# Kernel optimization log

Hardware: AMD Instinct MI355X
Metric: run time of the kernel (lower is better)

Reference implementation:

```python
import jax, jax.numpy as jnp
import numpy as np

NEG_SLOPE = 0.01  # F.leaky_relu / nn.LeakyReLU default

def _leaky(x):
    return jnp.where(x >= 0, x, NEG_SLOPE * x)

def _cgconv(x, src, dst, edge_attr, Wf, bf, Ws, bs):
    # PyG CGConv: z = [x_i, x_j, e]; msg = sigmoid(lin_f(z)) * softplus(lin_s(z)); out = x + scatter_add(msg, i)
    z = jnp.concatenate([x[dst], x[src], edge_attr], axis=-1)  # [E, 2C+D]
    m = jax.nn.sigmoid(z @ Wf + bf) * jax.nn.softplus(z @ Ws + bs)  # [E, C]
    agg = jax.ops.segment_sum(m, dst, num_segments=x.shape[0])
    return x + agg

def setup_inputs() -> dict:
    key = jax.random.key(0)
    ks = jax.random.split(key, 16)
    N, E, C, D, NC, G = 50000, 800000, 128, 32, 10, 64
    inp = {}
    inp['x'] = jax.random.normal(ks[0], (N, C), dtype=jnp.float32)
    inp['y'] = jax.random.randint(ks[1], (G,), 0, NC)
    inp['edge_index'] = jax.random.randint(ks[2], (2, E), 0, N)
    inp['edge_attr'] = jax.random.normal(ks[3], (E, D), dtype=jnp.float32)
    inp['batch'] = jnp.sort(jax.random.randint(ks[4], (N,), 0, G))
    s = 0.05
    inp['lin_W'] = jax.random.normal(ks[5], (C + NC, C), dtype=jnp.float32) * s
    inp['lin_b'] = jnp.zeros((C,), dtype=jnp.float32)
    inp['c1_Wf'] = jax.random.normal(ks[6], (2 * C + D, C), dtype=jnp.float32) * s
    inp['c1_bf'] = jnp.zeros((C,), dtype=jnp.float32)
    inp['c1_Ws'] = jax.random.normal(ks[7], (2 * C + D, C), dtype=jnp.float32) * s
    inp['c1_bs'] = jnp.zeros((C,), dtype=jnp.float32)
    inp['c2_Wf'] = jax.random.normal(ks[8], (2 * C + D, C), dtype=jnp.float32) * s
    inp['c2_bf'] = jnp.zeros((C,), dtype=jnp.float32)
    inp['c2_Ws'] = jax.random.normal(ks[9], (2 * C + D, C), dtype=jnp.float32) * s
    inp['c2_bs'] = jnp.zeros((C,), dtype=jnp.float32)
    inp['fc1_W'] = jax.random.normal(ks[10], (C + NC, 32), dtype=jnp.float32) * s
    inp['fc1_b'] = jnp.zeros((32,), dtype=jnp.float32)
    inp['fc2_W'] = jax.random.normal(ks[11], (32, 1), dtype=jnp.float32) * s
    inp['fc2_b'] = jnp.zeros((1,), dtype=jnp.float32)
    return inp

def reference(x, y, edge_index, edge_attr, batch, lin_W, lin_b, c1_Wf, c1_bf, c1_Ws, c1_bs, c2_Wf, c2_bf, c2_Ws, c2_bs, fc1_W, fc1_b, fc2_W, fc2_b):
    NC = fc1_W.shape[0] - c1_Wf.shape[1]  # n_classes = 10
    G = y.shape[0]
    src, dst = edge_index[0], edge_index[1]
    one_hot = jax.nn.one_hot(y[batch], NC, dtype=x.dtype)  # [N, NC]
    h = _leaky(jnp.concatenate([x, one_hot], axis=1) @ lin_W + lin_b)
    h = _leaky(_cgconv(h, src, dst, edge_attr, c1_Wf, c1_bf, c1_Ws, c1_bs))
    h = _cgconv(h, src, dst, edge_attr, c2_Wf, c2_bf, c2_Ws, c2_bs)
    h = jnp.concatenate([h, one_hot], axis=1)  # [N, C+NC]
    sums = jax.ops.segment_sum(h, batch, num_segments=G)
    cnts = jax.ops.segment_sum(jnp.ones((h.shape[0],), h.dtype), batch, num_segments=G)
    pooled = sums / jnp.maximum(cnts, 1.0)[:, None]  # global_mean_pool
    out = _leaky(pooled @ fc1_W + fc1_b) @ fc2_W + fc2_b
    return jax.nn.sigmoid(out)
```

## Files before the change

kernel.cpp:

```cpp
#include <hip/hip_runtime.h>
#include <hip/hip_bf16.h>
#include <math.h>

#define CCH 128
#define DK  32
#define NCLS 10

typedef __attribute__((ext_vector_type(2))) float f32x2;

__device__ __forceinline__ float leaky_f(float v) { return v >= 0.f ? v : 0.01f * v; }

__device__ __forceinline__ f32x2 gate2(f32x2 gf, f32x2 gs) {
  float sgx = 1.f / (1.f + __expf(-gf.x));
  float sgy = 1.f / (1.f + __expf(-gf.y));
  float spx = fmaxf(gs.x, 0.f) + __logf(1.f + __expf(-fabsf(gs.x)));
  float spy = fmaxf(gs.y, 0.f) + __logf(1.f + __expf(-fabsf(gs.y)));
  f32x2 r = {sgx * spx, sgy * spy};
  return r;
}

__global__ void k_hist(const int* __restrict__ dst, int* __restrict__ cnt, int E) {
  int e = blockIdx.x * 256 + threadIdx.x;
  if (e < E) atomicAdd(&cnt[dst[e]], 1);
}

__global__ void k_scan(const int* __restrict__ cnt, int* __restrict__ off,
                       int* __restrict__ cur, int N) {
  __shared__ int wsum[16];
  __shared__ int carry_s;
  int t = threadIdx.x;
  int lane = t & 63, w = t >> 6;
  if (t == 0) carry_s = 0;
  __syncthreads();
  for (int base = 0; base < N; base += 1024) {
    int i = base + t;
    int carry = carry_s;
    int v = (i < N) ? cnt[i] : 0;
    int s = v;
    #pragma unroll
    for (int d = 1; d < 64; d <<= 1) {
      int tmp = __shfl_up(s, d);
      if (lane >= d) s += tmp;
    }
    if (lane == 63) wsum[w] = s;
    __syncthreads();
    if (t < 16) {
      int u = wsum[t];
      #pragma unroll
      for (int d = 1; d < 16; d <<= 1) {
        int tmp = __shfl_up(u, d);
        if (t >= d) u += tmp;
      }
      wsum[t] = u;
      if (t == 15) carry_s = carry + u;
    }
    __syncthreads();
    int wbase = carry + (w > 0 ? wsum[w - 1] : 0);
    int excl = wbase + s - v;
    if (i < N) { off[i] = excl; cur[i] = excl; }
    __syncthreads();
  }
  if (t == 0) off[N] = carry_s;
}

__global__ void k_fill(const int* __restrict__ dst, const int* __restrict__ srcArr,
                       int* __restrict__ cur, int* __restrict__ eid,
                       int* __restrict__ esrc, int E) {
  int e = blockIdx.x * 256 + threadIdx.x;
  if (e < E) {
    int p = atomicAdd(&cur[dst[e]], 1);
    eid[p] = e;
    esrc[p] = srcArr[e];
  }
}

__global__ void k_gea(const int* __restrict__ eid, const float* __restrict__ ea,
                      float* __restrict__ ea_csr, int E) {
  int t = blockIdx.x * 256 + threadIdx.x;
  if (t >= E * 8) return;
  int i = t >> 3, q = t & 7;
  int e = eid[i];
  *(float4*)&ea_csr[(size_t)i * DK + q * 4] =
      *(const float4*)&ea[(size_t)e * DK + q * 4];
}

__global__ __launch_bounds__(256) void k_embed(
    const float* __restrict__ x, const float* __restrict__ lin_W,
    const float* __restrict__ lin_b, const int* __restrict__ batch,
    const int* __restrict__ y, float* __restrict__ h, int M) {
  __shared__ float Al[32 * 128];
  __shared__ float Wl[32 * 128];
  int t = threadIdx.x;
  int row0 = blockIdx.x * 32;
  for (int i = t * 4; i < 32 * 128; i += 1024) {
    int r = i >> 7, k = i & 127;
    int gr = row0 + r;
    float4 v = {0.f, 0.f, 0.f, 0.f};
    if (gr < M) v = *(const float4*)&x[(size_t)gr * 128 + k];
    *(float4*)&Al[i] = v;
  }
  int c4 = (t & 31) * 4;
  int rb = (t >> 5) * 4;
  float acc[4][4] = {};
  for (int ks = 0; ks < 128; ks += 32) {
    __syncthreads();
    for (int i = t * 4; i < 32 * 128; i += 1024)
      *(float4*)&Wl[i] = *(const float4*)&lin_W[(size_t)ks * 128 + i];
    __syncthreads();
    for (int k = 0; k < 32; k += 4) {
      float4 a[4];
      #pragma unroll
      for (int r = 0; r < 4; ++r) a[r] = *(float4*)&Al[(rb + r) * 128 + ks + k];
      #pragma unroll
      for (int kk = 0; kk < 4; ++kk) {
        float4 w = *(float4*)&Wl[(k + kk) * 128 + c4];
        #pragma unroll
        for (int r = 0; r < 4; ++r) {
          float av = kk == 0 ? a[r].x : kk == 1 ? a[r].y : kk == 2 ? a[r].z : a[r].w;
          acc[r][0] = fmaf(av, w.x, acc[r][0]);
          acc[r][1] = fmaf(av, w.y, acc[r][1]);
          acc[r][2] = fmaf(av, w.z, acc[r][2]);
          acc[r][3] = fmaf(av, w.w, acc[r][3]);
        }
      }
    }
  }
  #pragma unroll
  for (int r = 0; r < 4; ++r) {
    int gr = row0 + rb + r;
    if (gr < M) {
      int cls = y[batch[gr]];
      const float* wrow = &lin_W[(size_t)(128 + cls) * 128];
      float4 o;
      o.x = leaky_f(acc[r][0] + lin_b[c4 + 0] + wrow[c4 + 0]);
      o.y = leaky_f(acc[r][1] + lin_b[c4 + 1] + wrow[c4 + 1]);
      o.z = leaky_f(acc[r][2] + lin_b[c4 + 2] + wrow[c4 + 2]);
      o.w = leaky_f(acc[r][3] + lin_b[c4 + 3] + wrow[c4 + 3]);
      *(float4*)&h[(size_t)gr * 128 + c4] = o;
    }
  }
}

__global__ __launch_bounds__(256) void k_proj(
    const float* __restrict__ h, const float* __restrict__ Wf,
    const float* __restrict__ Ws, float* __restrict__ P, int M) {
  __shared__ float Al[32 * 128];
  __shared__ float Wl[32 * 128];
  int t = threadIdx.x;
  int part = blockIdx.y;
  const float* Wsrc = (part < 2 ? Wf : Ws) + (size_t)(part & 1) * (128 * 128);
  int row0 = blockIdx.x * 32;
  for (int i = t * 4; i < 32 * 128; i += 1024) {
    int r = i >> 7, k = i & 127;
    int gr = row0 + r;
    float4 v = {0.f, 0.f, 0.f, 0.f};
    if (gr < M) v = *(const float4*)&h[(size_t)gr * 128 + k];
    *(float4*)&Al[i] = v;
  }
  int c4 = (t & 31) * 4;
  int rb = (t >> 5) * 4;
  float acc[4][4] = {};
  for (int ks = 0; ks < 128; ks += 32) {
    __syncthreads();
    for (int i = t * 4; i < 32 * 128; i += 1024)
      *(float4*)&Wl[i] = *(const float4*)&Wsrc[(size_t)ks * 128 + i];
    __syncthreads();
    for (int k = 0; k < 32; k += 4) {
      float4 a[4];
      #pragma unroll
      for (int r = 0; r < 4; ++r) a[r] = *(float4*)&Al[(rb + r) * 128 + ks + k];
      #pragma unroll
      for (int kk = 0; kk < 4; ++kk) {
        float4 w = *(float4*)&Wl[(k + kk) * 128 + c4];
        #pragma unroll
        for (int r = 0; r < 4; ++r) {
          float av = kk == 0 ? a[r].x : kk == 1 ? a[r].y : kk == 2 ? a[r].z : a[r].w;
          acc[r][0] = fmaf(av, w.x, acc[r][0]);
          acc[r][1] = fmaf(av, w.y, acc[r][1]);
          acc[r][2] = fmaf(av, w.z, acc[r][2]);
          acc[r][3] = fmaf(av, w.w, acc[r][3]);
        }
      }
    }
  }
  #pragma unroll
  for (int r = 0; r < 4; ++r) {
    int gr = row0 + rb + r;
    if (gr < M) {
      float4 o = {acc[r][0], acc[r][1], acc[r][2], acc[r][3]};
      *(float4*)&P[(size_t)gr * 512 + part * 128 + c4] = o;
    }
  }
}

__global__ __launch_bounds__(256, 8)
void k_agg(
    const float* __restrict__ hin, const float* __restrict__ P,
    const int* __restrict__ off,
    const int* __restrict__ esrcArr, const float* __restrict__ ea_csr,
    const float* __restrict__ Wf, const float* __restrict__ Ws,
    const float* __restrict__ bfv, const float* __restrict__ bsv,
    float* __restrict__ hout, int N, int do_leaky) {
  __shared__ float WlF[32 * 128];
  __shared__ float WlS[32 * 128];
  int t = threadIdx.x;
  for (int i = t * 4; i < 32 * 128; i += 1024) {
    *(float4*)&WlF[i] = *(const float4*)&Wf[(size_t)256 * 128 + i];
    *(float4*)&WlS[i] = *(const float4*)&Ws[(size_t)256 * 128 + i];
  }
  __syncthreads();
  int lane = t & 63;
  int wave = __builtin_amdgcn_readfirstlane(t >> 6);
  int gw = blockIdx.x * 4 + wave;
  int c2 = lane * 2;
  f32x2 bf2 = *(const f32x2*)&bfv[c2];
  f32x2 bs2 = *(const f32x2*)&bsv[c2];
  int nstreams = gridDim.x * 4;
  for (int n = gw; n < N; n += nstreams) {
    int i0 = __builtin_amdgcn_readfirstlane(off[n]);
    int i1 = __builtin_amdgcn_readfirstlane(off[n + 1]);
    f32x2 acc = *(const f32x2*)&hin[(size_t)n * 128 + c2];
    f32x2 gf0 = *(const f32x2*)&P[(size_t)n * 512 + c2] + bf2;
    f32x2 gs0 = *(const f32x2*)&P[(size_t)n * 512 + 256 + c2] + bs2;
    #pragma unroll 1
    for (int i = i0; i < i1; ++i) {
      int s = __builtin_amdgcn_readfirstlane(esrcArr[i]);
      f32x2 gf = gf0 + *(const f32x2*)&P[(size_t)s * 512 + 128 + c2];
      f32x2 gs = gs0 + *(const f32x2*)&P[(size_t)s * 512 + 384 + c2];
      const float* e0 = ea_csr + (size_t)i * DK;
      #pragma unroll
      for (int q = 0; q < 4; ++q) {
        float4 a = *(const float4*)&e0[q * 8];
        float4 b = *(const float4*)&e0[q * 8 + 4];
        float ekk[8] = {a.x, a.y, a.z, a.w, b.x, b.y, b.z, b.w};
        #pragma unroll
        for (int j = 0; j < 8; ++j) {
          int k = q * 8 + j;
          f32x2 wfk = *(const f32x2*)&WlF[k * 128 + c2];
          f32x2 wsk = *(const f32x2*)&WlS[k * 128 + c2];
          f32x2 e2 = {ekk[j], ekk[j]};
          gf += e2 * wfk;
          gs += e2 * wsk;
        }
      }
      acc += gate2(gf, gs);
    }
    if (do_leaky) { acc.x = leaky_f(acc.x); acc.y = leaky_f(acc.y); }
    *(f32x2*)&hout[(size_t)n * 128 + c2] = acc;
  }
}

__device__ __forceinline__ int lbound(const int* a, int n, int key) {
  int lo = 0, hi = n;
  while (lo < hi) { int m = (lo + hi) >> 1; if (a[m] < key) lo = m + 1; else hi = m; }
  return lo;
}

__global__ void k_pool(const float* __restrict__ h, const int* __restrict__ batch,
                       float* __restrict__ pooled, int* __restrict__ gcnt, int N) {
  int g = blockIdx.x;
  int sidx = blockIdx.y, sgrid = gridDim.y;
  int t = threadIdx.x;
  int lo = lbound(batch, N, g);
  int hi = lbound(batch, N, g + 1);
  int len = hi - lo;
  if (sidx == 0 && t == 0) gcnt[g] = len;
  int per = (len + sgrid - 1) / sgrid;
  int a = lo + sidx * per;
  int b = min(hi, a + per);
  if (a >= b) return;
  float s = 0.f;
  for (int n = a; n < b; ++n) s += h[(size_t)n * 128 + t];
  atomicAdd(&pooled[g * 128 + t], s);
}

__global__ void k_fc(const float* __restrict__ pooled, const int* __restrict__ gcnt,
                     const int* __restrict__ y,
                     const float* __restrict__ W1, const float* __restrict__ b1,
                     const float* __restrict__ W2, const float* __restrict__ b2,
                     float* __restrict__ out) {
  int g = blockIdx.x;
  int j = threadIdx.x;
  float v = 0.f;
  if (j < 32) {
    int cnt = gcnt[g];
    float dot = 0.f;
    for (int k = 0; k < 128; ++k) dot = fmaf(pooled[g * 128 + k], W1[k * 32 + j], dot);
    float a = b1[j] + (cnt > 0 ? dot / (float)cnt + W1[(128 + y[g]) * 32 + j] : 0.f);
    a = leaky_f(a);
    v = a * W2[j];
  }
  #pragma unroll
  for (int o = 32; o > 0; o >>= 1) v += __shfl_down(v, o);
  if (j == 0) out[g] = 1.f / (1.f + __expf(-(v + b2[0])));
}

extern "C" void kernel_launch(void* const* d_in, const int* in_sizes, int n_in,
                              void* d_out, int out_size, void* d_ws, size_t ws_size,
                              hipStream_t stream) {
  const float* x        = (const float*)d_in[0];
  const int*   y        = (const int*)d_in[1];
  const int*   eidx     = (const int*)d_in[2];
  const float* ea       = (const float*)d_in[3];
  const int*   batch    = (const int*)d_in[4];
  const float* lin_W    = (const float*)d_in[5];
  const float* lin_b    = (const float*)d_in[6];
  const float* c1_Wf    = (const float*)d_in[7];
  const float* c1_bf    = (const float*)d_in[8];
  const float* c1_Ws    = (const float*)d_in[9];
  const float* c1_bs    = (const float*)d_in[10];
  const float* c2_Wf    = (const float*)d_in[11];
  const float* c2_bf    = (const float*)d_in[12];
  const float* c2_Ws    = (const float*)d_in[13];
  const float* c2_bs    = (const float*)d_in[14];
  const float* fc1_W    = (const float*)d_in[15];
  const float* fc1_b    = (const float*)d_in[16];
  const float* fc2_W    = (const float*)d_in[17];
  const float* fc2_b    = (const float*)d_in[18];
  float* out = (float*)d_out;

  const int N = in_sizes[0] / 128;
  const int G = in_sizes[1];
  const int E = in_sizes[2] / 2;
  const int* src = eidx;
  const int* dst = eidx + E;

  char* w = (char*)d_ws;
  float* P  = (float*)w;  w += (size_t)N * 512 * 4;
  float* hA = (float*)w;  w += (size_t)N * 128 * 4;
  float* hB = (float*)w;  w += (size_t)N * 128 * 4;
  float* pooled = (float*)w; w += (size_t)G * 128 * 4;
  int* gcnt = (int*)w; w += ((size_t)G * 4 + 15) & ~(size_t)15;
  int* cnt = (int*)w; w += (size_t)N * 4;
  int* off = (int*)w; w += ((size_t)(N + 1) * 4 + 15) & ~(size_t)15;
  int* eid = (int*)w; w += (size_t)E * 4;
  int* esrc = (int*)w; w += (size_t)E * 4;
  float* ea_csr = (float*)w; w += (size_t)E * DK * 4;

  hipMemsetAsync(cnt, 0, (size_t)N * 4, stream);
  hipMemsetAsync(pooled, 0, (size_t)G * 128 * 4, stream);
  k_hist<<<(E + 255) / 256, 256, 0, stream>>>(dst, cnt, E);
  k_scan<<<1, 1024, 0, stream>>>(cnt, off, cnt , N);
  k_fill<<<(E + 255) / 256, 256, 0, stream>>>(dst, src, cnt, eid, esrc, E);
  k_gea<<<(E * 8 + 255) / 256, 256, 0, stream>>>(eid, ea, ea_csr, E);

  k_embed<<<(N + 31) / 32, 256, 0, stream>>>(x, lin_W, lin_b, batch, y, hA, N);

  k_proj<<<dim3((N + 31) / 32, 4), 256, 0, stream>>>(hA, c1_Wf, c1_Ws, P, N);
  k_agg<<<2048, 256, 0, stream>>>(hA, P, off, esrc, ea_csr, c1_Wf, c1_Ws, c1_bf, c1_bs, hB, N, 1);

  k_proj<<<dim3((N + 31) / 32, 4), 256, 0, stream>>>(hB, c2_Wf, c2_Ws, P, N);
  k_agg<<<2048, 256, 0, stream>>>(hB, P, off, esrc, ea_csr, c2_Wf, c2_Ws, c2_bf, c2_bs, hA, N, 0);

  k_pool<<<dim3(G, 8), 128, 0, stream>>>(hA, batch, pooled, gcnt, N);
  k_fc<<<G, 64, 0, stream>>>(pooled, gcnt, y, fc1_W, fc1_b, fc2_W, fc2_b, out);
}
```

Before: 1.240 ms.

## Interleave source-gate projections and prefetch next neighbor row in aggregation

The projection kernel now writes the two source-side gate projections (filter and softplus) interleaved in one 256-float block, so each edge reads a single float4 per lane instead of two separate f32x2 gathers. The aggregation loop software-prefetches the next edge's gathered row, splits the edge-attribute dot product into two independent accumulator chains, and uses nontemporal loads and stores for streaming edge attributes and node features. The occupancy hint of 8 waves per SIMD is dropped from launch bounds, which may raise register use and lower occupancy. The aim is to hide gather latency and improve memory coalescing in the edge loop.

Result: no change. 1.237 ms (-0.2%).

```diff
diff --git a/kernel.cpp b/kernel.cpp
--- a/kernel.cpp
+++ b/kernel.cpp
@@ -7,6 +7,7 @@
 #define NCLS 10
 
 typedef __attribute__((ext_vector_type(2))) float f32x2;
+typedef __attribute__((ext_vector_type(4))) float f32x4;
 
 __device__ __forceinline__ float leaky_f(float v) { return v >= 0.f ? v : 0.01f * v; }
 
@@ -187,13 +188,25 @@
   for (int r = 0; r < 4; ++r) {
     int gr = row0 + rb + r;
     if (gr < M) {
-      float4 o = {acc[r][0], acc[r][1], acc[r][2], acc[r][3]};
-      *(float4*)&P[(size_t)gr * 512 + part * 128 + c4] = o;
-    }
-  }
-}
-
-__global__ __launch_bounds__(256, 8)
+      float* Pn = P + (size_t)gr * 512;
+      if (part == 0) {
+        float4 o = {acc[r][0], acc[r][1], acc[r][2], acc[r][3]};
+        *(float4*)&Pn[c4] = o;
+      } else if (part == 2) {
+        float4 o = {acc[r][0], acc[r][1], acc[r][2], acc[r][3]};
+        *(float4*)&Pn[128 + c4] = o;
+      } else {
+        int pbase = 256 + (c4 >> 1) * 4 + (part == 3 ? 2 : 0);
+        f32x2 lo = {acc[r][0], acc[r][1]};
+        f32x2 hi = {acc[r][2], acc[r][3]};
+        *(f32x2*)&Pn[pbase] = lo;
+        *(f32x2*)&Pn[pbase + 4] = hi;
+      }
+    }
+  }
+}
+
+__global__ __launch_bounds__(256)
 void k_agg(
     const float* __restrict__ hin, const float* __restrict__ P,
     const int* __restrict__ off,
@@ -219,34 +232,43 @@
   for (int n = gw; n < N; n += nstreams) {
     int i0 = __builtin_amdgcn_readfirstlane(off[n]);
     int i1 = __builtin_amdgcn_readfirstlane(off[n + 1]);
-    f32x2 acc = *(const f32x2*)&hin[(size_t)n * 128 + c2];
+    f32x2 acc = __builtin_nontemporal_load((const f32x2*)&hin[(size_t)n * 128 + c2]);
     f32x2 gf0 = *(const f32x2*)&P[(size_t)n * 512 + c2] + bf2;
-    f32x2 gs0 = *(const f32x2*)&P[(size_t)n * 512 + 256 + c2] + bs2;
-    #pragma unroll 1
-    for (int i = i0; i < i1; ++i) {
-      int s = __builtin_amdgcn_readfirstlane(esrcArr[i]);
-      f32x2 gf = gf0 + *(const f32x2*)&P[(size_t)s * 512 + 128 + c2];
-      f32x2 gs = gs0 + *(const f32x2*)&P[(size_t)s * 512 + 384 + c2];
-      const float* e0 = ea_csr + (size_t)i * DK;
-      #pragma unroll
-      for (int q = 0; q < 4; ++q) {
-        float4 a = *(const float4*)&e0[q * 8];
-        float4 b = *(const float4*)&e0[q * 8 + 4];
-        float ekk[8] = {a.x, a.y, a.z, a.w, b.x, b.y, b.z, b.w};
+    f32x2 gs0 = *(const f32x2*)&P[(size_t)n * 512 + 128 + c2] + bs2;
+    if (i0 < i1) {
+      int sP = __builtin_amdgcn_readfirstlane(esrcArr[i0]);
+      f32x4 bP = *(const f32x4*)&P[(size_t)sP * 512 + 256 + lane * 4];
+      #pragma unroll 1
+      for (int i = i0; i < i1; ++i) {
+        f32x4 b = bP;
+        int inx = i + 1 < i1 ? i + 1 : i;
+        int sN = __builtin_amdgcn_readfirstlane(esrcArr[inx]);
+        bP = *(const f32x4*)&P[(size_t)sN * 512 + 256 + lane * 4];
+        f32x2 gfA = gf0 + (f32x2){b.x, b.y};
+        f32x2 gsA = gs0 + (f32x2){b.z, b.w};
+        f32x2 gfB = {0.f, 0.f};
+        f32x2 gsB = {0.f, 0.f};
+        const float* e0 = ea_csr + (size_t)i * DK;
         #pragma unroll
-        for (int j = 0; j < 8; ++j) {
-          int k = q * 8 + j;
-          f32x2 wfk = *(const f32x2*)&WlF[k * 128 + c2];
-          f32x2 wsk = *(const f32x2*)&WlS[k * 128 + c2];
-          f32x2 e2 = {ekk[j], ekk[j]};
-          gf += e2 * wfk;
-          gs += e2 * wsk;
+        for (int q = 0; q < 4; ++q) {
+          f32x4 a = __builtin_nontemporal_load((const f32x4*)&e0[q * 8]);
+          f32x4 c = __builtin_nontemporal_load((const f32x4*)&e0[q * 8 + 4]);
+          float ekk[8] = {a.x, a.y, a.z, a.w, c.x, c.y, c.z, c.w};
+          #pragma unroll
+          for (int j = 0; j < 8; ++j) {
+            int k = q * 8 + j;
+            f32x2 wfk = *(const f32x2*)&WlF[k * 128 + c2];
+            f32x2 wsk = *(const f32x2*)&WlS[k * 128 + c2];
+            f32x2 e2 = {ekk[j], ekk[j]};
+            if (q < 2) { gfA += e2 * wfk; gsA += e2 * wsk; }
+            else       { gfB += e2 * wfk; gsB += e2 * wsk; }
+          }
         }
-      }
-      acc += gate2(gf, gs);
+        acc += gate2(gfA + gfB, gsA + gsB);
+      }
     }
     if (do_leaky) { acc.x = leaky_f(acc.x); acc.y = leaky_f(acc.y); }
-    *(f32x2*)&hout[(size_t)n * 128 + c2] = acc;
+    __builtin_nontemporal_store(acc, (f32x2*)&hout[(size_t)n * 128 + c2]);
   }
 }
 
```
